# Kernel optimization log

Hardware: AMD Instinct MI355X
Metric: run time of the kernel (lower is better)

Reference implementation:

```python
import jax, jax.numpy as jnp
import numpy as np

DIM = 512
HEADS = 8
DIM_HEAD = 64
HIDDEN = HEADS * DIM_HEAD  # 512
SCALE = DIM_HEAD ** -0.5


def setup_inputs() -> dict:
    key = jax.random.key(0)
    k1, k2, k3, k4 = jax.random.split(key, 4)
    B, N = 8, 4096
    x = jax.random.normal(k1, (B, DIM, N), dtype=jnp.float32)
    # Conv1d with kernel_size=1, no bias -> weight [out, in]
    w_qkv = jax.random.normal(k2, (HIDDEN * 3, DIM), dtype=jnp.float32) * (DIM ** -0.5)
    w_out = jax.random.normal(k3, (DIM, HIDDEN), dtype=jnp.float32) * (HIDDEN ** -0.5)
    b_out = jax.random.normal(k4, (DIM,), dtype=jnp.float32) * 0.01
    return {"x": x, "w_qkv": w_qkv, "w_out": w_out, "b_out": b_out}


def reference(x, w_qkv, w_out, b_out):
    B, _, N = x.shape
    # pointwise conv1d == channel GEMM: [3*hidden, dim] x [b, dim, n]
    qkv = jnp.einsum('oi,bin->bon', w_qkv, x)
    q, k, v = jnp.split(qkv, 3, axis=1)
    # b (h c) n -> b h c n
    reshape = lambda t: t.reshape(B, HEADS, DIM_HEAD, N)
    q, k, v = reshape(q), reshape(k), reshape(v)
    q = q * SCALE
    k = jax.nn.softmax(k, axis=-1)  # softmax over sequence dim n
    # context: [b h d e] = sum_n k[b h d n] v[b h e n]
    context = jnp.einsum('bhdn,bhen->bhde', k, v)
    # out: [b h e n] = sum_d context[b h d e] q[b h d n]
    out = jnp.einsum('bhde,bhdn->bhen', context, q)
    out = out.reshape(B, HIDDEN, N)  # b (h e) n
    return jnp.einsum('oi,bin->bon', w_out, out) + b_out[None, :, None]
```

## Files before the change

kernel.cpp:

```cpp
#include <hip/hip_runtime.h>
#include <hip/hip_bf16.h>
#include <cstdint>

typedef unsigned short u16;
typedef __attribute__((ext_vector_type(8))) short bf16x8;
typedef __attribute__((ext_vector_type(4))) float f32x4;

__device__ __forceinline__ u16 f2b(float f) {
  union { float f; unsigned u; } x; x.f = f;
  unsigned r = x.u + 0x7fffu + ((x.u >> 16) & 1u);
  return (u16)(r >> 16);
}
__device__ __forceinline__ float b2f(u16 u) {
  union { unsigned u; float f; } x; x.u = ((unsigned)u) << 16;
  return x.f;
}
__device__ __forceinline__ void gld16(void* lds, const void* g) {
  __builtin_amdgcn_global_load_lds((const __attribute__((address_space(1))) void*)g,
                                   (__attribute__((address_space(3))) void*)lds, 16, 0, 0);
}
__device__ __forceinline__ int sw_idx(int n, int c) {
  return n * 64 + ((((c >> 2) ^ (n >> 2)) & 15) << 2) + (c & 3);
}
__device__ __forceinline__ int ekb(int row, int c2) {
  return (row * 256 + c2) ^ ((((row >> 3) ^ row) & 7) << 4);
}

__global__ __launch_bounds__(256) void pre(const float* __restrict__ x,
                                           u16* __restrict__ xt,
                                           const float* __restrict__ w_qkv,
                                           u16* __restrict__ wkvh,
                                           u16* __restrict__ wqT,
                                           float* __restrict__ zbuf) {
  __shared__ u16 t[4096];
  const int tid = threadIdx.x;
  const int blk = blockIdx.x;
  if (blk < 4096) {
    const int b = blk >> 9;
    const int c0 = ((blk >> 6) & 7) * 64;
    const int n0 = (blk & 63) * 64;
    const int nl = (tid & 15) * 4;
    const int cl = tid >> 4;
#pragma unroll
    for (int r = 0; r < 4; r++) {
      const int c = cl + r * 16;
      const float4 v = *(const float4*)(x + ((long)b * 512 + c0 + c) * 4096 + n0 + nl);
      t[sw_idx(nl + 0, c)] = f2b(v.x);
      t[sw_idx(nl + 1, c)] = f2b(v.y);
      t[sw_idx(nl + 2, c)] = f2b(v.z);
      t[sw_idx(nl + 3, c)] = f2b(v.w);
    }
    __syncthreads();
    const int cw = (tid & 15) * 4;
#pragma unroll
    for (int r = 0; r < 4; r++) {
      const int n = cl + r * 16;
      const u16* tp = &t[sw_idx(n, cw)];
      ushort4 o; o.x = tp[0]; o.y = tp[1]; o.z = tp[2]; o.w = tp[3];
      *(ushort4*)(xt + ((long)b * 4096 + n0 + n) * 512 + c0 + cw) = o;
    }
    return;
  }
  const int pblk = blk - 4096;
  if (pblk < 512) {
    const int i = pblk * 1024 + tid * 4;
    const int ri = i >> 9;
    const int col = i & 511;
    const int h = (ri >> 6) & 7;
    const int orow = h * 128 + ((ri >> 9) << 6) + (ri & 63);
    const float4 v = *(const float4*)(w_qkv + 262144 + i);
    ushort4 r; r.x = f2b(v.x); r.y = f2b(v.y); r.z = f2b(v.z); r.w = f2b(v.w);
    *(ushort4*)(wkvh + orow * 512 + col) = r;
  } else if (pblk < 576) {
    const int bb = pblk - 512;
    const int i0 = (bb & 7) * 64;
    const int c0 = (bb >> 3) * 64;
    const int il = (tid & 15) * 4;
    const int cl = tid >> 4;
#pragma unroll
    for (int r = 0; r < 4; r++) {
      const int c = cl + r * 16;
      const float4 v = *(const float4*)(w_qkv + (c0 + c) * 512 + i0 + il);
      t[sw_idx(il + 0, c)] = f2b(v.x);
      t[sw_idx(il + 1, c)] = f2b(v.y);
      t[sw_idx(il + 2, c)] = f2b(v.z);
      t[sw_idx(il + 3, c)] = f2b(v.w);
    }
    __syncthreads();
    const int cw = (tid & 15) * 4;
#pragma unroll
    for (int r = 0; r < 4; r++) {
      const int i = cl + r * 16;
      const u16* tp = &t[sw_idx(i, cw)];
      ushort4 o; o.x = tp[0]; o.y = tp[1]; o.z = tp[2]; o.w = tp[3];
      *(ushort4*)(wqT + (i0 + i) * 512 + c0 + cw) = o;
    }
  } else {
    const int zi = (pblk - 576) * 1024 + tid * 4;
    if (zi < 266240) *(float4*)(zbuf + zi) = float4{0.f, 0.f, 0.f, 0.f};
  }
}

__global__ __launch_bounds__(256, 4) void kvctx(const u16* __restrict__ wkvh,
                                                const u16* __restrict__ xt,
                                                float* __restrict__ ctx,
                                                float* __restrict__ rsum) {
  __shared__ u16 sh[16384];
  u16* As = sh;
  u16* Bs = sh + 8192;
  u16* Ek = sh;
  u16* Vs = sh + 8192;

  const int tid = threadIdx.x;
  const int wid = tid >> 6;
  const int lane = tid & 63;
  const int wm = wid >> 1, wn = wid & 1;

  const int flat = blockIdx.x;
  const int xcd = flat & 7;
  const int slot = flat >> 3;
  const int h = slot & 7;
  const int tile = xcd * 32 + (slot >> 3);
  const int nc = tile & 31;
  const int b = tile >> 5;
  const int bh = b * 8 + h;

  const u16* Ab = wkvh + (long)h * 128 * 512;
  const u16* Bb = xt + ((long)b * 4096 + (long)nc * 128) * 512;
  const int q8 = (lane >> 4) * 8;
  const int mr = lane & 15;
  const int quad = lane >> 4;
  const int m7 = mr & 7;

  f32x4 acc[4][4] = {};

  for (int kk = 0; kk < 512; kk += 64) {
    __syncthreads();
#pragma unroll
    for (int i = 0; i < 4; i++) {
      const int slot2 = i * 256 + tid;
      const int row = slot2 >> 3;
      const int kc = ((slot2 & 7) ^ (row & 7)) * 8;
      gld16((char*)As + i * 4096 + wid * 1024, Ab + (long)row * 512 + kk + kc);
      gld16((char*)Bs + i * 4096 + wid * 1024, Bb + (long)row * 512 + kk + kc);
    }
    __syncthreads();
#pragma unroll
    for (int ks = 0; ks < 2; ks++) {
      bf16x8 af[4], bfv[4];
#pragma unroll
      for (int i = 0; i < 4; i++)
        af[i] = *(const bf16x8*)(As + (wm * 64 + i * 16 + mr) * 64 +
                                 (((ks * 4 + quad) ^ m7) * 8));
#pragma unroll
      for (int j = 0; j < 4; j++)
        bfv[j] = *(const bf16x8*)(Bs + (wn * 64 + j * 16 + mr) * 64 +
                                  (((ks * 4 + quad) ^ m7) * 8));
#pragma unroll
      for (int i = 0; i < 4; i++)
#pragma unroll
        for (int j = 0; j < 4; j++)
          acc[i][j] = __builtin_amdgcn_mfma_f32_16x16x32_bf16(af[i], bfv[j], acc[i][j], 0, 0, 0);
    }
  }

  __syncthreads();
  u16* dst = (wm == 0) ? Ek : Vs;
#pragma unroll
  for (int i = 0; i < 4; i++) {
#pragma unroll
    for (int r = 0; r < 4; r++) {
      const int row = i * 16 + quad * 4 + r;
      float sloc = 0.f;
#pragma unroll
      for (int j = 0; j < 4; j++) {
        float v = acc[i][j][r];
        if (wm == 0) v = __expf(v);
        const u16 bv = f2b(v);
        const int col = wn * 64 + j * 16 + mr;
        *(u16*)((char*)dst + ekb(row, col * 2)) = bv;
        if (wm == 0) sloc += b2f(bv);
      }
      if (wm == 0) {
        sloc += __shfl_xor(sloc, 1);
        sloc += __shfl_xor(sloc, 2);
        sloc += __shfl_xor(sloc, 4);
        sloc += __shfl_xor(sloc, 8);
        if (mr == 0) atomicAdd(rsum + (long)bh * 64 + row, sloc);
      }
    }
  }
  __syncthreads();

  f32x4 acc2[2][2] = {};
#pragma unroll
  for (int ks = 0; ks < 4; ks++) {
    bf16x8 ef[2], vf[2];
#pragma unroll
    for (int ii = 0; ii < 2; ii++) {
      const int row = wm * 32 + ii * 16 + mr;
      ef[ii] = *(const bf16x8*)((const char*)Ek + ekb(row, (ks * 32 + q8) * 2));
    }
#pragma unroll
    for (int jj = 0; jj < 2; jj++) {
      const int row = wn * 32 + jj * 16 + mr;
      vf[jj] = *(const bf16x8*)((const char*)Vs + ekb(row, (ks * 32 + q8) * 2));
    }
#pragma unroll
    for (int ii = 0; ii < 2; ii++)
#pragma unroll
      for (int jj = 0; jj < 2; jj++)
        acc2[ii][jj] = __builtin_amdgcn_mfma_f32_16x16x32_bf16(ef[ii], vf[jj], acc2[ii][jj], 0, 0, 0);
  }

  float* cb = ctx + (long)bh * 4096;
#pragma unroll
  for (int ii = 0; ii < 2; ii++)
#pragma unroll
    for (int jj = 0; jj < 2; jj++)
#pragma unroll
      for (int r = 0; r < 4; r++) {
        const int d = wm * 32 + ii * 16 + quad * 4 + r;
        const int e = wn * 32 + jj * 16 + mr;
        atomicAdd(cb + d * 64 + e, acc2[ii][jj][r]);
      }
}

__global__ __launch_bounds__(256) void wc_kern(const float* __restrict__ ctxp,
                                               const float* __restrict__ rsump,
                                               const float* __restrict__ wout,
                                               u16* __restrict__ Wc) {
  __shared__ float cs[64 * 65];
  __shared__ float rinv[64];
  const int tid = threadIdx.x;
  const int bh = blockIdx.x, og = blockIdx.y;
  const int b = bh >> 3, h = bh & 7;
  if (tid < 64) rinv[tid] = 1.0f / rsump[(long)bh * 64 + tid];
  __syncthreads();
  for (int i = tid; i < 4096; i += 256) {
    const int d = i >> 6, e = i & 63;
    cs[e * 65 + d] = ctxp[(long)bh * 4096 + i] * rinv[d];
  }
  __syncthreads();
  const int d = tid & 63;
  const int o0 = og * 32 + (tid >> 6) * 8;
  float csr[64];
#pragma unroll
  for (int e = 0; e < 64; e++) csr[e] = cs[e * 65 + d];
  u16* wcp = Wc + (long)b * 512 * 512;
  for (int rr = 0; rr < 8; rr++) {
    const int o = o0 + rr;
    const float* wrow = wout + (long)o * 512 + h * 64;
    float a0 = 0.f, a1 = 0.f, a2 = 0.f, a3 = 0.f;
#pragma unroll
    for (int e = 0; e < 64; e += 4) {
      a0 += wrow[e + 0] * csr[e + 0];
      a1 += wrow[e + 1] * csr[e + 1];
      a2 += wrow[e + 2] * csr[e + 2];
      a3 += wrow[e + 3] * csr[e + 3];
    }
    wcp[(long)o * 512 + h * 64 + d] = f2b((a0 + a1) + (a2 + a3));
  }
}

__global__ __launch_bounds__(256) void weff_gemm(const u16* __restrict__ Wc,
                                                 const u16* __restrict__ wqT,
                                                 u16* __restrict__ Weff) {
  __shared__ u16 As[64 * 64];
  __shared__ u16 Bs[64 * 64];
  const int tid = threadIdx.x;
  const int wid = tid >> 6;
  const int lane = tid & 63;
  const int wm = wid >> 1, wn = wid & 1;
  const int gn = blockIdx.x, gm = blockIdx.y, b = blockIdx.z;

  const u16* Ab = Wc + (long)b * 512 * 512 + (long)gm * 64 * 512;
  const u16* Bb = wqT + (long)gn * 64 * 512;

  f32x4 acc[2][2] = {};
  const int mr = lane & 15;
  const int quad = lane >> 4;
  const int m7 = mr & 7;

  for (int kk = 0; kk < 512; kk += 64) {
    __syncthreads();
#pragma unroll
    for (int i = 0; i < 2; i++) {
      const int slot = i * 256 + tid;
      const int row = slot >> 3;
      const int kc = ((slot & 7) ^ (row & 7)) * 8;
      gld16((char*)As + i * 4096 + wid * 1024, Ab + (long)row * 512 + kk + kc);
      gld16((char*)Bs + i * 4096 + wid * 1024, Bb + (long)row * 512 + kk + kc);
    }
    __syncthreads();
#pragma unroll
    for (int ks = 0; ks < 2; ks++) {
      bf16x8 af[2], bfv[2];
#pragma unroll
      for (int i = 0; i < 2; i++)
        af[i] = *(const bf16x8*)(As + (wm * 32 + i * 16 + mr) * 64 +
                                 (((ks * 4 + quad) ^ m7) * 8));
#pragma unroll
      for (int j = 0; j < 2; j++)
        bfv[j] = *(const bf16x8*)(Bs + (wn * 32 + j * 16 + mr) * 64 +
                                  (((ks * 4 + quad) ^ m7) * 8));
#pragma unroll
      for (int i = 0; i < 2; i++)
#pragma unroll
        for (int j = 0; j < 2; j++)
          acc[i][j] = __builtin_amdgcn_mfma_f32_16x16x32_bf16(af[i], bfv[j], acc[i][j], 0, 0, 0);
    }
  }

  const int col = lane & 15;
  u16* wb = Weff + (long)b * 512 * 512;
#pragma unroll
  for (int i = 0; i < 2; i++)
#pragma unroll
    for (int r = 0; r < 4; r++) {
      const int grow = gm * 64 + wm * 32 + i * 16 + quad * 4 + r;
#pragma unroll
      for (int j = 0; j < 2; j++) {
        const int gcol = gn * 64 + wn * 32 + j * 16 + col;
        wb[(long)grow * 512 + gcol] = f2b(acc[i][j][r] * 0.125f);
      }
    }
}

__global__ __launch_bounds__(256) void out_gemm(const u16* __restrict__ Weff,
                                                const u16* __restrict__ xt,
                                                const float* __restrict__ bias,
                                                float* __restrict__ outp) {
  __shared__ u16 As[128 * 64];
  __shared__ u16 Bs[128 * 64];
  const int tid = threadIdx.x;
  const int wid = tid >> 6;
  const int lane = tid & 63;
  const int wm = wid >> 1, wn = wid & 1;
  const int gn = blockIdx.x, gm = blockIdx.y, b = blockIdx.z;

  const u16* Ab = Weff + (long)b * 512 * 512 + (long)gm * 128 * 512;
  const u16* Bb = xt + ((long)b * 4096 + (long)gn * 128) * 512;

  f32x4 acc[4][4] = {};
  const int mr = lane & 15;
  const int quad = lane >> 4;
  const int m7 = mr & 7;

  for (int kk = 0; kk < 512; kk += 64) {
    __syncthreads();
#pragma unroll
    for (int i = 0; i < 4; i++) {
      const int slot = i * 256 + tid;
      const int row = slot >> 3;
      const int kc = ((slot & 7) ^ (row & 7)) * 8;
      gld16((char*)As + i * 4096 + wid * 1024, Ab + (long)row * 512 + kk + kc);
      gld16((char*)Bs + i * 4096 + wid * 1024, Bb + (long)row * 512 + kk + kc);
    }
    __syncthreads();
#pragma unroll
    for (int ks = 0; ks < 2; ks++) {
      bf16x8 af[4], bfv[4];
#pragma unroll
      for (int i = 0; i < 4; i++)
        af[i] = *(const bf16x8*)(As + (wm * 64 + i * 16 + mr) * 64 +
                                 (((ks * 4 + quad) ^ m7) * 8));
#pragma unroll
      for (int j = 0; j < 4; j++)
        bfv[j] = *(const bf16x8*)(Bs + (wn * 64 + j * 16 + mr) * 64 +
                                  (((ks * 4 + quad) ^ m7) * 8));
#pragma unroll
      for (int i = 0; i < 4; i++)
#pragma unroll
        for (int j = 0; j < 4; j++)
          acc[i][j] = __builtin_amdgcn_mfma_f32_16x16x32_bf16(af[i], bfv[j], acc[i][j], 0, 0, 0);
    }
  }

  const int col = lane & 15;
#pragma unroll
  for (int i = 0; i < 4; i++)
#pragma unroll
    for (int r = 0; r < 4; r++) {
      const int grow = gm * 128 + wm * 64 + i * 16 + quad * 4 + r;
      const float bv = bias[grow];
#pragma unroll
      for (int j = 0; j < 4; j++) {
        const long gcol = (long)gn * 128 + wn * 64 + j * 16 + col;
        outp[((long)b * 512 + grow) * 4096 + gcol] = acc[i][j][r] + bv;
      }
    }
}

extern "C" void kernel_launch(void* const* d_in, const int* in_sizes, int n_in,
                              void* d_out, int out_size, void* d_ws, size_t ws_size,
                              hipStream_t stream) {
  const float* x = (const float*)d_in[0];
  const float* w_qkv = (const float*)d_in[1];
  const float* w_out = (const float*)d_in[2];
  const float* b_out = (const float*)d_in[3];
  float* out = (float*)d_out;
  char* ws = (char*)d_ws;

  u16* xt = (u16*)(ws + 0);
  u16* wkvh = (u16*)(ws + 33554432);
  u16* wqT = (u16*)(ws + 34603008);
  u16* wc = (u16*)(ws + 35127296);
  u16* weff = (u16*)(ws + 39321600);
  float* ctx = (float*)(ws + 43515904);
  float* rsum = (float*)(ws + 44564480);

  pre<<<4932, 256, 0, stream>>>(x, xt, w_qkv, wkvh, wqT, ctx);
  kvctx<<<2048, 256, 0, stream>>>(wkvh, xt, ctx, rsum);
  wc_kern<<<dim3(64, 16), 256, 0, stream>>>(ctx, rsum, w_out, wc);
  weff_gemm<<<dim3(8, 8, 8), 256, 0, stream>>>(wc, wqT, weff);
  out_gemm<<<dim3(32, 4, 8), 256, 0, stream>>>(weff, xt, b_out, out);
}
```

Before: 242.8 us.

## Double-buffer kvctx LDS tiles and widen block to eight waves

The kvctx kernel moves from 4 to 8 waves per block, so each wave computes a 64x32 slice of the KV projection instead of 64x64. The K-loop now double-buffers the A/B tiles in 64KB of LDS, issuing the next stage's async global-to-LDS loads before computing on the current buffer, and drops one barrier per iteration. This is meant to hide load latency and raise MFMA concurrency. The cost is lower occupancy from the larger LDS footprint and block size, and each wave keeps a smaller register tile.

```diff
diff --git a/kernel.cpp b/kernel.cpp
--- a/kernel.cpp
+++ b/kernel.cpp
@@ -101,20 +101,19 @@
   }
 }
 
-__global__ __launch_bounds__(256, 4) void kvctx(const u16* __restrict__ wkvh,
-                                                const u16* __restrict__ xt,
-                                                float* __restrict__ ctx,
-                                                float* __restrict__ rsum) {
-  __shared__ u16 sh[16384];
-  u16* As = sh;
-  u16* Bs = sh + 8192;
+__global__ __launch_bounds__(512) void kvctx(const u16* __restrict__ wkvh,
+                                             const u16* __restrict__ xt,
+                                             float* __restrict__ ctx,
+                                             float* __restrict__ rsum) {
+  __shared__ u16 sh[32768];
   u16* Ek = sh;
   u16* Vs = sh + 8192;
 
   const int tid = threadIdx.x;
   const int wid = tid >> 6;
   const int lane = tid & 63;
-  const int wm = wid >> 1, wn = wid & 1;
+  const int wm = wid >> 2;
+  const int wn = wid & 3;
 
   const int flat = blockIdx.x;
   const int xcd = flat & 7;
@@ -127,39 +126,46 @@
 
   const u16* Ab = wkvh + (long)h * 128 * 512;
   const u16* Bb = xt + ((long)b * 4096 + (long)nc * 128) * 512;
-  const int q8 = (lane >> 4) * 8;
   const int mr = lane & 15;
   const int quad = lane >> 4;
+  const int q8 = quad * 8;
   const int m7 = mr & 7;
 
-  f32x4 acc[4][4] = {};
-
-  for (int kk = 0; kk < 512; kk += 64) {
-    __syncthreads();
-#pragma unroll
-    for (int i = 0; i < 4; i++) {
-      const int slot2 = i * 256 + tid;
-      const int row = slot2 >> 3;
-      const int kc = ((slot2 & 7) ^ (row & 7)) * 8;
-      gld16((char*)As + i * 4096 + wid * 1024, Ab + (long)row * 512 + kk + kc);
-      gld16((char*)Bs + i * 4096 + wid * 1024, Bb + (long)row * 512 + kk + kc);
-    }
-    __syncthreads();
+  f32x4 acc[4][2] = {};
+
+  auto stage = [&](int buf, int kk) {
+    char* base = (char*)sh + buf * 32768;
+#pragma unroll
+    for (int i = 0; i < 2; i++) {
+      const int s = i * 512 + tid;
+      const int row = s >> 3;
+      const int kc = ((s & 7) ^ (row & 7)) * 8;
+      char* d = base + i * 8192 + wid * 1024;
+      gld16(d, Ab + (long)row * 512 + kk + kc);
+      gld16(d + 16384, Bb + (long)row * 512 + kk + kc);
+    }
+  };
+
+  stage(0, 0);
+  for (int t = 0; t < 8; t++) {
+    __syncthreads();
+    if (t < 7) stage((t + 1) & 1, (t + 1) * 64);
+    const u16* As = sh + (t & 1) * 16384;
+    const u16* Bs = As + 8192;
 #pragma unroll
     for (int ks = 0; ks < 2; ks++) {
-      bf16x8 af[4], bfv[4];
+      bf16x8 af[4], bfv[2];
+      const int rc = ((ks * 4 + quad) ^ m7) * 8;
 #pragma unroll
       for (int i = 0; i < 4; i++)
-        af[i] = *(const bf16x8*)(As + (wm * 64 + i * 16 + mr) * 64 +
-                                 (((ks * 4 + quad) ^ m7) * 8));
-#pragma unroll
-      for (int j = 0; j < 4; j++)
-        bfv[j] = *(const bf16x8*)(Bs + (wn * 64 + j * 16 + mr) * 64 +
-                                  (((ks * 4 + quad) ^ m7) * 8));
+        af[i] = *(const bf16x8*)(As + (wm * 64 + i * 16 + mr) * 64 + rc);
+#pragma unroll
+      for (int j = 0; j < 2; j++)
+        bfv[j] = *(const bf16x8*)(Bs + (wn * 32 + j * 16 + mr) * 64 + rc);
 #pragma unroll
       for (int i = 0; i < 4; i++)
 #pragma unroll
-        for (int j = 0; j < 4; j++)
+        for (int j = 0; j < 2; j++)
           acc[i][j] = __builtin_amdgcn_mfma_f32_16x16x32_bf16(af[i], bfv[j], acc[i][j], 0, 0, 0);
     }
   }
@@ -173,11 +179,11 @@
       const int row = i * 16 + quad * 4 + r;
       float sloc = 0.f;
 #pragma unroll
-      for (int j = 0; j < 4; j++) {
+      for (int j = 0; j < 2; j++) {
         float v = acc[i][j][r];
         if (wm == 0) v = __expf(v);
         const u16 bv = f2b(v);
-        const int col = wn * 64 + j * 16 + mr;
+        const int col = wn * 32 + j * 16 + mr;
         *(u16*)((char*)dst + ekb(row, col * 2)) = bv;
         if (wm == 0) sloc += b2f(bv);
       }
@@ -192,38 +198,33 @@
   }
   __syncthreads();
 
-  f32x4 acc2[2][2] = {};
+  f32x4 acc2[2] = {};
 #pragma unroll
   for (int ks = 0; ks < 4; ks++) {
-    bf16x8 ef[2], vf[2];
+    bf16x8 ef[2], vf;
 #pragma unroll
     for (int ii = 0; ii < 2; ii++) {
       const int row = wm * 32 + ii * 16 + mr;
       ef[ii] = *(const bf16x8*)((const char*)Ek + ekb(row, (ks * 32 + q8) * 2));
     }
-#pragma unroll
-    for (int jj = 0; jj < 2; jj++) {
-      const int row = wn * 32 + jj * 16 + mr;
-      vf[jj] = *(const bf16x8*)((const char*)Vs + ekb(row, (ks * 32 + q8) * 2));
+    {
+      const int row = wn * 16 + mr;
+      vf = *(const bf16x8*)((const char*)Vs + ekb(row, (ks * 32 + q8) * 2));
     }
 #pragma unroll
     for (int ii = 0; ii < 2; ii++)
-#pragma unroll
-      for (int jj = 0; jj < 2; jj++)
-        acc2[ii][jj] = __builtin_amdgcn_mfma_f32_16x16x32_bf16(ef[ii], vf[jj], acc2[ii][jj], 0, 0, 0);
+      acc2[ii] = __builtin_amdgcn_mfma_f32_16x16x32_bf16(ef[ii], vf, acc2[ii], 0, 0, 0);
   }
 
   float* cb = ctx + (long)bh * 4096;
 #pragma unroll
   for (int ii = 0; ii < 2; ii++)
 #pragma unroll
-    for (int jj = 0; jj < 2; jj++)
-#pragma unroll
-      for (int r = 0; r < 4; r++) {
-        const int d = wm * 32 + ii * 16 + quad * 4 + r;
-        const int e = wn * 32 + jj * 16 + mr;
-        atomicAdd(cb + d * 64 + e, acc2[ii][jj][r]);
-      }
+    for (int r = 0; r < 4; r++) {
+      const int d = wm * 32 + ii * 16 + quad * 4 + r;
+      const int e = wn * 16 + mr;
+      atomicAdd(cb + d * 64 + e, acc2[ii][r]);
+    }
 }
 
 __global__ __launch_bounds__(256) void wc_kern(const float* __restrict__ ctxp,
@@ -411,7 +412,7 @@
   float* rsum = (float*)(ws + 44564480);
 
   pre<<<4932, 256, 0, stream>>>(x, xt, w_qkv, wkvh, wqT, ctx);
-  kvctx<<<2048, 256, 0, stream>>>(wkvh, xt, ctx, rsum);
+  kvctx<<<2048, 512, 0, stream>>>(wkvh, xt, ctx, rsum);
   wc_kern<<<dim3(64, 16), 256, 0, stream>>>(ctx, rsum, w_out, wc);
   weff_gemm<<<dim3(8, 8, 8), 256, 0, stream>>>(wc, wqT, weff);
   out_gemm<<<dim3(32, 4, 8), 256, 0, stream>>>(weff, xt, b_out, out);
```

Measured after the change: 248.4 us. 1.02x slower.
